# Performance work log

Measured on AMD Instinct MI355X. Metric: run time of the kernel, lower is better.

## Reference

```python
import jax, jax.numpy as jnp
import numpy as np
from jax import lax

T, B, D, H, L, NDIR = 512, 64, 512, 512, 3, 2

def _lengths():
    return 512 - 4 * np.arange(64)  # per-sequence lengths, non-increasing

def _qdq(w):
    # simulate dynamic int8 symmetric per-tensor weight quantization
    s = jnp.max(jnp.abs(w)) / 127.0
    return jnp.clip(jnp.round(w / s), -127, 127) * s

def setup_inputs() -> dict:
    key = jax.random.key(0)
    ks = jax.random.split(key, 9)
    lengths = _lengths()
    bs = np.array([(lengths > t).sum() for t in range(T)], dtype=np.int64)  # [T]
    pack_idx = np.concatenate([t * B + np.arange(bs[t]) for t in range(T)]).astype(np.int32)
    sc = 0.05
    data = jax.random.normal(ks[0], (int(bs.sum()), D), jnp.float32)
    h0 = jax.random.normal(ks[1], (L * NDIR, B, H), jnp.float32)
    c0 = jax.random.normal(ks[2], (L * NDIR, B, H), jnp.float32)
    w_ih0 = _qdq(jax.random.normal(ks[3], (NDIR, 4 * H, D)) * sc)
    w_hh0 = _qdq(jax.random.normal(ks[4], (NDIR, 4 * H, H)) * sc)
    b0 = jax.random.normal(ks[5], (NDIR, 4 * H)) * sc  # b_ih + b_hh combined
    w_ih_r = _qdq(jax.random.normal(ks[6], (L - 1, NDIR, 4 * H, NDIR * H)) * sc)
    w_hh_r = _qdq(jax.random.normal(ks[7], (L - 1, NDIR, 4 * H, H)) * sc)
    b_r = jax.random.normal(ks[8], (L - 1, NDIR, 4 * H)) * sc
    return {"data": data, "h0": h0, "c0": c0, "w_ih0": w_ih0, "w_hh0": w_hh0, "b0": b0,
            "w_ih_r": w_ih_r, "w_hh_r": w_hh_r, "b_r": b_r,
            "batch_sizes": jnp.asarray(bs), "pack_idx": jnp.asarray(pack_idx)}

def _run_dir(x, mask, h0, c0, w_ih, w_hh, b):
    # x: [T,B,in], mask: [T,B]; batch the input GEMM over all timesteps
    gx = jnp.einsum('tbd,gd->tbg', x, w_ih) + b  # [T,B,4H]
    def step(carry, inp):
        h, c = carry
        gx_t, m = inp
        gates = gx_t + h @ w_hh.T
        i, f, g, o = jnp.split(gates, 4, axis=-1)  # PyTorch gate order i,f,g,o
        c_new = jax.nn.sigmoid(f) * c + jax.nn.sigmoid(i) * jnp.tanh(g)
        h_new = jax.nn.sigmoid(o) * jnp.tanh(c_new)
        m = m[:, None]
        return (jnp.where(m, h_new, h), jnp.where(m, c_new, c)), jnp.where(m, h_new, h)
    (hT, cT), ys = lax.scan(step, (h0, c0), (gx, mask))
    return ys * mask[:, :, None], hT, cT

def _lstm(data, h0, c0, w_ih0, w_hh0, b0, w_ih_r, w_hh_r, b_r, batch_sizes, pack_idx):
    mask = jnp.arange(B)[None, :] < batch_sizes[:, None]          # [T,B] valid slots
    lengths = jnp.sum(mask, axis=0)                                # [B]
    rev_idx = jnp.clip(lengths[None, :] - 1 - jnp.arange(T)[:, None], 0, T - 1)  # [T,B]
    barange = jnp.arange(B)[None, :]
    x = jnp.zeros((T * B, D), data.dtype).at[pack_idx].set(data).reshape(T, B, D)
    h_ns, c_ns = [], []
    for l in range(L):
        outs = []
        for d in range(NDIR):
            if l == 0:
                w_ih, w_hh, b = w_ih0[d], w_hh0[d], b0[d]
            else:
                w_ih, w_hh, b = w_ih_r[l - 1, d], w_hh_r[l - 1, d], b_r[l - 1, d]
            hi, ci = h0[NDIR * l + d], c0[NDIR * l + d]
            if d == 0:
                ys, hT, cT = _run_dir(x, mask, hi, ci, w_ih, w_hh, b)
            else:
                x_rev = x[rev_idx, barange]               # per-sequence reversal
                ys_r, hT, cT = _run_dir(x_rev, mask, hi, ci, w_ih, w_hh, b)
                ys = ys_r[rev_idx, barange] * mask[:, :, None]
            outs.append(ys); h_ns.append(hT); c_ns.append(cT)
        x = jnp.concatenate(outs, axis=-1)  # [T,B,2H] feeds next layer
    out = x.reshape(T * B, NDIR * H)[pack_idx]  # repack to [total_tokens, 2H]
    return out, jnp.stack(h_ns), jnp.stack(c_ns)

def reference(data, h0, c0, w_ih0, w_hh0, b0, w_ih_r, w_hh_r, b_r, batch_sizes, pack_idx):
    return _lstm(data, h0, c0, w_ih0, w_hh0, b0, w_ih_r, w_hh_r, b_r, batch_sizes, pack_idx)
```

## Files before the change

### kernel.cpp

```cpp
#include <hip/hip_runtime.h>
#include <cmath>

typedef _Float16 f16;
typedef _Float16 half8 __attribute__((ext_vector_type(8)));
typedef float floatx4 __attribute__((ext_vector_type(4)));
typedef unsigned u32x4 __attribute__((ext_vector_type(4)));

#define NT 512
#define NB 64
#define NH 512
#define NG 2048
#define CHUNK 128

__device__ inline float sigf(float x) { return 1.0f / (1.0f + __expf(-x)); }
__device__ inline float tanhfast(float x) { return 2.0f / (1.0f + __expf(-2.0f * x)) - 1.0f; }

__device__ inline void load_lds16(const f16* g, f16* l) {
  __builtin_amdgcn_global_load_lds(
      (__attribute__((address_space(1))) void*)g,
      (__attribute__((address_space(3))) void*)l, 16, 0, 0);
}

__global__ void prep_meta(const int* __restrict__ bs_raw, int* __restrict__ lens,
                          int* __restrict__ cum) {
  __shared__ int sbs[NT];
  int stride = (bs_raw[1] == 0) ? 2 : 1;
  for (int i = threadIdx.x; i < NT; i += 256) sbs[i] = bs_raw[i * stride];
  __syncthreads();
  for (int b = threadIdx.x; b < NB; b += 256) {
    int n = 0;
    for (int t = 0; t < NT; ++t) n += (sbs[t] > b);
    lens[b] = n;
  }
  if (threadIdx.x == 0) {
    int run = 0;
    for (int t = 0; t < NT; ++t) { cum[t] = run; run += sbs[t]; }
  }
}

__global__ void scatter_rows(const float* __restrict__ data, const int* __restrict__ pidx,
                             f16* __restrict__ X0) {
  int r = blockIdx.x;
  int row = pidx[r];
  const float* src = data + (size_t)r * 512;
  f16* dst = X0 + (size_t)row * 512;
  for (int k = threadIdx.x; k < 512; k += 256) dst[k] = (f16)src[k];
}

__global__ void f32_to_f16(const float* __restrict__ in, f16* __restrict__ out, size_t n) {
  size_t i = (size_t)blockIdx.x * 256 + threadIdx.x;
  size_t stride = (size_t)gridDim.x * 256;
  for (; i < n; i += stride) out[i] = (f16)in[i];
}

__global__ void init_h(const float* __restrict__ h0, const float* __restrict__ c0,
                       float* __restrict__ hsave, float* __restrict__ csave,
                       unsigned* __restrict__ ht, unsigned* __restrict__ ctr, int layer) {
  int idx = blockIdx.x * 256 + threadIdx.x;
  int d = idx >> 15, rem = idx & 32767;
  float hv = h0[(size_t)(2 * layer + d) * NB * NH + rem];
  float cv = c0[(size_t)(2 * layer + d) * NB * NH + rem];
  hsave[idx] = hv;
  csave[idx] = cv;
  union { f16 f; unsigned short s; } hc; hc.f = (f16)hv;
  unsigned word = ((unsigned)(layer * NT) << 16) | hc.s;
  __hip_atomic_store(ht + (size_t)d * NB * NH + rem, word,
                     __ATOMIC_RELAXED, __HIP_MEMORY_SCOPE_AGENT);
  if (blockIdx.x == 0) {
    __hip_atomic_store(ctr + threadIdx.x, (unsigned)(layer * NT),
                       __ATOMIC_RELAXED, __HIP_MEMORY_SCOPE_AGENT);
  }
}

__device__ void gemm_body(const f16* __restrict__ A, const f16* __restrict__ W,
                          const float* __restrict__ bias, const int* __restrict__ lens,
                          f16* __restrict__ gxc, int K, int c0, int id) {
  const int d = id >> 10;
  const int m0 = ((id >> 4) & 63) * 128;
  const int n0 = (id & 15) * 128;
  const f16* Wd = W + (size_t)d * NG * K;

  __shared__ __align__(16) f16 As[128 * 32];
  __shared__ __align__(16) f16 Bs[128 * 32];

  const int tid = threadIdx.x, lane = tid & 63, wv = tid >> 6;
  const int wm = wv >> 1, wn = wv & 1;
  const int lrow = lane >> 2, lcol = (lane & 3) * 8;
  const int q = lane >> 4, nn = lane & 15;

  const f16* aptr[2];
  const f16* bptr[2];
#pragma unroll
  for (int i = 0; i < 2; ++i) {
    int ch = wv * 2 + i;
    int m = m0 + ch * 16 + lrow;
    int t = c0 + (m >> 6), b = m & 63;
    int tt = t;
    if (d) { tt = lens[b] - 1 - t; tt = tt < 0 ? 0 : (tt > NT - 1 ? NT - 1 : tt); }
    aptr[i] = A + (size_t)(tt * NB + b) * K + lcol;
    bptr[i] = Wd + (size_t)(n0 + ch * 16 + lrow) * K + lcol;
  }

  floatx4 acc[4][4] = {};
  for (int k0 = 0; k0 < K; k0 += 32) {
    __syncthreads();
#pragma unroll
    for (int i = 0; i < 2; ++i) {
      int ch = wv * 2 + i;
      load_lds16(aptr[i] + k0, As + ch * 512);
      load_lds16(bptr[i] + k0, Bs + ch * 512);
    }
    __syncthreads();
    half8 a[4], b[4];
#pragma unroll
    for (int f = 0; f < 4; ++f) {
      a[f] = *(const half8*)(As + (wm * 64 + f * 16 + nn) * 32 + q * 8);
      b[f] = *(const half8*)(Bs + (wn * 64 + f * 16 + nn) * 32 + q * 8);
    }
#pragma unroll
    for (int fm = 0; fm < 4; ++fm)
#pragma unroll
      for (int fn = 0; fn < 4; ++fn)
        acc[fm][fn] = __builtin_amdgcn_mfma_f32_16x16x32_f16(a[fm], b[fn], acc[fm][fn], 0, 0, 0);
  }

  f16* gxd = gxc + (size_t)d * CHUNK * NB * NG;
#pragma unroll
  for (int fn = 0; fn < 4; ++fn) {
    int col = n0 + wn * 64 + fn * 16 + nn;
    float bv = bias[d * NG + col];
#pragma unroll
    for (int fm = 0; fm < 4; ++fm) {
      int mb = m0 + wm * 64 + fm * 16 + q * 4;
#pragma unroll
      for (int r = 0; r < 4; ++r)
        gxd[(size_t)(mb + r) * NG + col] = (f16)(acc[fm][fn][r] + bv);
    }
  }
}

__global__ __launch_bounds__(256) void gemm_gx(const f16* __restrict__ A,
                                               const f16* __restrict__ W,
                                               const float* __restrict__ bias,
                                               const int* __restrict__ lens,
                                               f16* __restrict__ gxc, int K, int c0) {
  gemm_body(A, W, bias, lens, gxc, K, c0,
            (int)(blockIdx.z * 1024 + blockIdx.y * 16 + blockIdx.x));
}

__global__ __launch_bounds__(256, 1) void lstm_rec(
    const f16* __restrict__ gxc, const f16* __restrict__ whh,
    const int* __restrict__ lens, const int* __restrict__ cum,
    float* __restrict__ hsave, float* __restrict__ csave,
    unsigned* __restrict__ ht, unsigned* __restrict__ ctr,
    f16* __restrict__ Y, float* __restrict__ outp,
    float* __restrict__ hT, float* __restrict__ cT,
    int c0, int mode, int layer,
    const f16* __restrict__ Xg, const f16* __restrict__ wih,
    const float* __restrict__ biasg, f16* __restrict__ gxn, int Kg, int c0n) {
  if (blockIdx.x >= 256) {
    if (gxn) gemm_body(Xg, wih, biasg, lens, gxn, Kg, c0n, (int)blockIdx.x - 256);
    return;
  }
  const int tid = threadIdx.x, lane = tid & 63, wv = tid >> 6;
  const int g = blockIdx.x & 7, w = blockIdx.x >> 3;
  const int dir = g & 1, bsl = g >> 1;
  const int q = lane >> 4, nn = lane & 15;

  const int maxlen = lens[bsl * 16];
  int nst = maxlen - c0;
  if (nst <= 0) return;
  if (nst > CHUNK) nst = CHUNK;

  __shared__ __align__(16) unsigned As[2][16][260];
  __shared__ float s_g[4][16][17];

  const int jbase = w * 16 + wv * 4;
  const int coln = (nn >> 2) * NH + jbase + (nn & 3);
  const f16* whd = whh + (size_t)dir * NG * NH;
  half8 bf[16];
#pragma unroll
  for (int s = 0; s < 16; ++s) {
    bf[s] = *(const half8*)(whd + (size_t)coln * NH + s * 32 + q * 8);
    asm volatile("" : "+v"(bf[s]));
  }

  const int b_e = bsl * 16 + nn;
  const int jglob = jbase + q;
  const int lene = lens[b_e];
  const int brow = bsl * 16 + q * 4;
  const int lidx = (dir * NB + b_e) * NH + jglob;
  float h = hsave[lidx], c = csave[lidx];

  const f16* gxd = gxc + (size_t)dir * CHUNK * NB * NG;
  const int ebase = layer * NT;

  const unsigned* cslot = ctr + (size_t)g * 32 + (lane & 31);

  for (int ct = 0; ct < nst; ++ct) {
    const int t = c0 + ct;
    const int e = ebase + t;
    const int par = t & 1;

    float gxv[4];
#pragma unroll
    for (int r = 0; r < 4; ++r)
      gxv[r] = (float)gxd[(size_t)(ct * NB + brow + r) * NG + coln];

    {
      const unsigned* cp = cslot + par * 256;
      int it = 0;
      for (;;) {
        unsigned cv = __hip_atomic_load(cp, __ATOMIC_RELAXED, __HIP_MEMORY_SCOPE_AGENT);
        if (__ballot((int)cv >= e) == ~0ull) break;
        if (++it > 200000) break;
        __builtin_amdgcn_s_sleep(1);
      }
    }

    const unsigned long long* p64 =
        (const unsigned long long*)(ht + ((size_t)(par * 2 + dir) * NB + bsl * 16 + nn) * NH +
                                    wv * 128 + q * 8);
    unsigned long long wb[16];
    {
      int it = 0;
      for (;;) {
#pragma unroll
        for (int i = 0; i < 16; ++i)
          wb[i] = __hip_atomic_load(p64 + (i >> 2) * 16 + (i & 3), __ATOMIC_RELAXED,
                                    __HIP_MEMORY_SCOPE_AGENT);
        unsigned tg = 0xffffu;
#pragma unroll
        for (int i = 0; i < 16; ++i) {
          tg &= (unsigned)(wb[i] >> 16) & 0xffffu;
          tg &= (unsigned)(wb[i] >> 48);
        }
        if (__ballot(tg >= (unsigned)e) == ~0ull) break;
        if (++it > 50000) break;
        __builtin_amdgcn_s_sleep(1);
      }
    }

#pragma unroll
    for (int s = 0; s < 4; ++s) {
      unsigned d0 = (unsigned)(wb[4 * s + 0] & 0xffffu) | ((unsigned)(wb[4 * s + 0] >> 32) << 16);
      unsigned d1 = (unsigned)(wb[4 * s + 1] & 0xffffu) | ((unsigned)(wb[4 * s + 1] >> 32) << 16);
      unsigned d2 = (unsigned)(wb[4 * s + 2] & 0xffffu) | ((unsigned)(wb[4 * s + 2] >> 32) << 16);
      unsigned d3 = (unsigned)(wb[4 * s + 3] & 0xffffu) | ((unsigned)(wb[4 * s + 3] >> 32) << 16);
      *(u32x4*)&As[par][nn][wv * 64 + s * 16 + q * 4] = (u32x4){d0, d1, d2, d3};
    }
    __syncthreads();

    floatx4 acc0 = {0.f, 0.f, 0.f, 0.f}, acc1 = {0.f, 0.f, 0.f, 0.f};
#pragma unroll
    for (int s = 0; s < 8; ++s) {
      half8 a0 = *(const half8*)&As[par][nn][(2 * s) * 16 + q * 4];
      half8 a1 = *(const half8*)&As[par][nn][(2 * s + 1) * 16 + q * 4];
      acc0 = __builtin_amdgcn_mfma_f32_16x16x32_f16(a0, bf[2 * s], acc0, 0, 0, 0);
      acc1 = __builtin_amdgcn_mfma_f32_16x16x32_f16(a1, bf[2 * s + 1], acc1, 0, 0, 0);
    }
#pragma unroll
    for (int r4 = 0; r4 < 4; ++r4) s_g[wv][q * 4 + r4][nn] = acc0[r4] + acc1[r4] + gxv[r4];

    const bool act = (t < lene);
    if (act) {
      float gi = s_g[wv][nn][q];
      float gf = s_g[wv][nn][4 + q];
      float gg = s_g[wv][nn][8 + q];
      float go = s_g[wv][nn][12 + q];
      c = sigf(gf) * c + sigf(gi) * tanhfast(gg);
      h = sigf(go) * tanhfast(c);
    }
    union { f16 f; unsigned short s; } hc; hc.f = (f16)h;
    unsigned word = ((unsigned)(e + 1) << 16) | hc.s;
    __hip_atomic_store(ht + ((size_t)(((t + 1) & 1) * 2 + dir) * NB + b_e) * NH + jglob,
                       word, __ATOMIC_RELAXED, __HIP_MEMORY_SCOPE_AGENT);
    if (tid == 0)
      __hip_atomic_store(ctr + (size_t)(((t + 1) & 1) * 256 + g * 32 + w), (unsigned)(e + 1),
                         __ATOMIC_RELAXED, __HIP_MEMORY_SCOPE_AGENT);
    if (mode == 0) {
      int tp = act ? (dir ? (lene - 1 - t) : t) : t;
      Y[(size_t)(tp * NB + b_e) * (2 * NH) + dir * NH + jglob] = act ? (f16)h : (f16)0.f;
    } else if (act) {
      int tp = dir ? (lene - 1 - t) : t;
      outp[(size_t)(cum[tp] + b_e) * (2 * NH) + dir * NH + jglob] = h;
    }
  }

  hsave[lidx] = h;
  csave[lidx] = c;
  const int sidx = ((2 * layer + dir) * NB + b_e) * NH + jglob;
  hT[sidx] = h;
  cT[sidx] = c;
}

extern "C" void kernel_launch(void* const* d_in, const int* in_sizes, int n_in,
                              void* d_out, int out_size, void* d_ws, size_t ws_size,
                              hipStream_t stream) {
  const float* data  = (const float*)d_in[0];
  const float* h0    = (const float*)d_in[1];
  const float* c0    = (const float*)d_in[2];
  const float* w_ih0 = (const float*)d_in[3];
  const float* w_hh0 = (const float*)d_in[4];
  const float* b0    = (const float*)d_in[5];
  const float* w_ihr = (const float*)d_in[6];
  const float* w_hhr = (const float*)d_in[7];
  const float* b_r   = (const float*)d_in[8];
  const int* bs_raw  = (const int*)d_in[9];
  const int* pidx    = (const int*)d_in[10];
  const int nrows = in_sizes[0] / 512;
  float* out = (float*)d_out;

  f16* Y0 = (f16*)d_out;
  float* hT = out + (size_t)nrows * 1024;
  float* cT = hT + (size_t)6 * NB * NH;

  char* p = (char*)d_ws;
  auto take = [&](size_t bytes) {
    char* r = p;
    p += (bytes + 255) & ~(size_t)255;
    return (void*)r;
  };
  const size_t gsz = (size_t)2 * CHUNK * NB * NG * 2;
  f16* gxcA  = (f16*)take(gsz);
  f16* Y1    = (f16*)take((size_t)NT * NB * 1024 * 2);
  f16* X0    = Y1;
  f16* wih16 = (f16*)take((size_t)2 * NG * 1024 * 2);
  f16* whh16 = (f16*)take((size_t)2 * NG * NH * 2);
  unsigned* ht = (unsigned*)take((size_t)2 * 2 * NB * NH * 4);
  unsigned* ctr = (unsigned*)take((size_t)2 * 8 * 32 * 4);
  float* hsave = (float*)take((size_t)2 * NB * NH * 4);
  float* csave = (float*)take((size_t)2 * NB * NH * 4);
  int* lens = (int*)take(256);
  int* cum  = (int*)take(NT * 4);
  f16* gxcB = nullptr;
  if ((size_t)(p - (char*)d_ws) + gsz <= ws_size) gxcB = (f16*)take(gsz);
  const bool fuse = (gxcB != nullptr);

  prep_meta<<<1, 256, 0, stream>>>(bs_raw, lens, cum);
  (void)hipMemsetAsync(X0, 0, (size_t)NT * NB * 512 * 2, stream);
  (void)hipMemsetAsync(ht, 0, (size_t)2 * 2 * NB * NH * 4, stream);
  (void)hipMemsetAsync(ctr, 0, (size_t)2 * 8 * 32 * 4, stream);
  scatter_rows<<<nrows, 256, 0, stream>>>(data, pidx, X0);

  for (int l = 0; l < 3; ++l) {
    const float* wih_f = (l == 0) ? w_ih0 : w_ihr + (size_t)(l - 1) * 2 * NG * 1024;
    const float* whh_f = (l == 0) ? w_hh0 : w_hhr + (size_t)(l - 1) * 2 * NG * NH;
    const float* bias  = (l == 0) ? b0 : b_r + (size_t)(l - 1) * 2 * NG;
    const int K = (l == 0) ? 512 : 1024;
    const f16* Xl = (l == 0) ? X0 : ((l == 1) ? Y0 : Y1);
    f16* Yl = (l == 0) ? Y0 : Y1;
    f32_to_f16<<<256, 256, 0, stream>>>(wih_f, wih16, (size_t)2 * NG * K);
    f32_to_f16<<<256, 256, 0, stream>>>(whh_f, whh16, (size_t)2 * NG * NH);
    init_h<<<256, 256, 0, stream>>>(h0, c0, hsave, csave, ht, ctr, l);
    for (int c = 0; c < 4; ++c) {
      f16* gcur = fuse ? ((c & 1) ? gxcB : gxcA) : gxcA;
      if (c == 0 || !fuse)
        gemm_gx<<<dim3(16, 64, 2), 256, 0, stream>>>(Xl, wih16, bias, lens, gcur, K, c * CHUNK);
      const bool g_on = fuse && (c < 3);
      f16* gnext = g_on ? (((c + 1) & 1) ? gxcB : gxcA) : nullptr;
      const int grid = g_on ? 2304 : 256;
      lstm_rec<<<grid, 256, 0, stream>>>(gcur, whh16, lens, cum, hsave, csave, ht, ctr, Yl,
                                         out, hT, cT, c * CHUNK, (l == 2) ? 1 : 0, l,
                                         Xl, wih16, bias, gnext, K, (c + 1) * CHUNK);
    }
  }
}
```

Measured before the change: 6.990 ms.

## Share LDS between recurrent and GEMM blocks, raise recurrent priority, fuse prep kernels

The recurrent kernel's fused GEMM tail blocks and the recurrent blocks now alias a single shared-memory buffer instead of separate static arrays. This lowers the per-block LDS footprint so more GEMM blocks can be co-resident with the recurrent blocks. Recurrent blocks raise their wave priority with s_setprio so the latency-critical recurrence is scheduled ahead of the overlapping GEMM work. The three per-layer prep kernels (two weight conversions and h/c init) are merged into one launch to cut launch overhead.

```diff
diff --git a/kernel.cpp b/kernel.cpp
--- a/kernel.cpp
+++ b/kernel.cpp
@@ -47,41 +47,41 @@
   for (int k = threadIdx.x; k < 512; k += 256) dst[k] = (f16)src[k];
 }
 
-__global__ void f32_to_f16(const float* __restrict__ in, f16* __restrict__ out, size_t n) {
-  size_t i = (size_t)blockIdx.x * 256 + threadIdx.x;
-  size_t stride = (size_t)gridDim.x * 256;
-  for (; i < n; i += stride) out[i] = (f16)in[i];
-}
-
-__global__ void init_h(const float* __restrict__ h0, const float* __restrict__ c0,
-                       float* __restrict__ hsave, float* __restrict__ csave,
-                       unsigned* __restrict__ ht, unsigned* __restrict__ ctr, int layer) {
-  int idx = blockIdx.x * 256 + threadIdx.x;
-  int d = idx >> 15, rem = idx & 32767;
-  float hv = h0[(size_t)(2 * layer + d) * NB * NH + rem];
-  float cv = c0[(size_t)(2 * layer + d) * NB * NH + rem];
-  hsave[idx] = hv;
-  csave[idx] = cv;
-  union { f16 f; unsigned short s; } hc; hc.f = (f16)hv;
-  unsigned word = ((unsigned)(layer * NT) << 16) | hc.s;
-  __hip_atomic_store(ht + (size_t)d * NB * NH + rem, word,
-                     __ATOMIC_RELAXED, __HIP_MEMORY_SCOPE_AGENT);
-  if (blockIdx.x == 0) {
-    __hip_atomic_store(ctr + threadIdx.x, (unsigned)(layer * NT),
+__global__ void prep_layer(const float* __restrict__ wih_f, f16* __restrict__ wih16, int n1,
+                           const float* __restrict__ whh_f, f16* __restrict__ whh16, int n2,
+                           const float* __restrict__ h0, const float* __restrict__ c0,
+                           float* __restrict__ hsave, float* __restrict__ csave,
+                           unsigned* __restrict__ ht, unsigned* __restrict__ ctr, int layer) {
+  int gid = blockIdx.x * 256 + threadIdx.x;
+  int stride = gridDim.x * 256;
+  for (int i = gid; i < n1; i += stride) wih16[i] = (f16)wih_f[i];
+  for (int i = gid; i < n2; i += stride) whh16[i] = (f16)whh_f[i];
+  for (int i = gid; i < 2 * NB * NH; i += stride) {
+    int d = i >> 15, rem = i & 32767;
+    float hv = h0[(size_t)(2 * layer + d) * NB * NH + rem];
+    float cv = c0[(size_t)(2 * layer + d) * NB * NH + rem];
+    hsave[i] = hv;
+    csave[i] = cv;
+    union { f16 f; unsigned short s; } hc; hc.f = (f16)hv;
+    unsigned word = ((unsigned)(layer * NT) << 16) | hc.s;
+    __hip_atomic_store(ht + (size_t)d * NB * NH + rem, word,
                        __ATOMIC_RELAXED, __HIP_MEMORY_SCOPE_AGENT);
   }
+  if (gid < 256)
+    __hip_atomic_store(ctr + gid, (unsigned)(layer * NT),
+                       __ATOMIC_RELAXED, __HIP_MEMORY_SCOPE_AGENT);
 }
 
 __device__ void gemm_body(const f16* __restrict__ A, const f16* __restrict__ W,
                           const float* __restrict__ bias, const int* __restrict__ lens,
-                          f16* __restrict__ gxc, int K, int c0, int id) {
+                          f16* __restrict__ gxc, int K, int c0, int id, char* sm) {
   const int d = id >> 10;
   const int m0 = ((id >> 4) & 63) * 128;
   const int n0 = (id & 15) * 128;
   const f16* Wd = W + (size_t)d * NG * K;
 
-  __shared__ __align__(16) f16 As[128 * 32];
-  __shared__ __align__(16) f16 Bs[128 * 32];
+  f16* As = (f16*)sm;
+  f16* Bs = (f16*)(sm + 8192);
 
   const int tid = threadIdx.x, lane = tid & 63, wv = tid >> 6;
   const int wm = wv >> 1, wn = wv & 1;
@@ -144,8 +144,9 @@
                                                const float* __restrict__ bias,
                                                const int* __restrict__ lens,
                                                f16* __restrict__ gxc, int K, int c0) {
+  __shared__ __align__(16) char gsm[16384];
   gemm_body(A, W, bias, lens, gxc, K, c0,
-            (int)(blockIdx.z * 1024 + blockIdx.y * 16 + blockIdx.x));
+            (int)(blockIdx.z * 1024 + blockIdx.y * 16 + blockIdx.x), gsm);
 }
 
 __global__ __launch_bounds__(256, 1) void lstm_rec(
@@ -158,10 +159,15 @@
     int c0, int mode, int layer,
     const f16* __restrict__ Xg, const f16* __restrict__ wih,
     const float* __restrict__ biasg, f16* __restrict__ gxn, int Kg, int c0n) {
+  __shared__ __align__(16) char smem[37632];
   if (blockIdx.x >= 256) {
-    if (gxn) gemm_body(Xg, wih, biasg, lens, gxn, Kg, c0n, (int)blockIdx.x - 256);
+    if (gxn) gemm_body(Xg, wih, biasg, lens, gxn, Kg, c0n, (int)blockIdx.x - 256, smem);
     return;
   }
+  __builtin_amdgcn_s_setprio(1);
+  unsigned (*As)[16][260] = (unsigned(*)[16][260])smem;
+  float (*s_g)[16][17] = (float(*)[16][17])(smem + 33280);
+
   const int tid = threadIdx.x, lane = tid & 63, wv = tid >> 6;
   const int g = blockIdx.x & 7, w = blockIdx.x >> 3;
   const int dir = g & 1, bsl = g >> 1;
@@ -171,9 +177,6 @@
   int nst = maxlen - c0;
   if (nst <= 0) return;
   if (nst > CHUNK) nst = CHUNK;
-
-  __shared__ __align__(16) unsigned As[2][16][260];
-  __shared__ float s_g[4][16][17];
 
   const int jbase = w * 16 + wv * 4;
   const int coln = (nn >> 2) * NH + jbase + (nn & 3);
@@ -350,9 +353,8 @@
     const int K = (l == 0) ? 512 : 1024;
     const f16* Xl = (l == 0) ? X0 : ((l == 1) ? Y0 : Y1);
     f16* Yl = (l == 0) ? Y0 : Y1;
-    f32_to_f16<<<256, 256, 0, stream>>>(wih_f, wih16, (size_t)2 * NG * K);
-    f32_to_f16<<<256, 256, 0, stream>>>(whh_f, whh16, (size_t)2 * NG * NH);
-    init_h<<<256, 256, 0, stream>>>(h0, c0, hsave, csave, ht, ctr, l);
+    prep_layer<<<512, 256, 0, stream>>>(wih_f, wih16, 2 * NG * K, whh_f, whh16,
+                                        2 * NG * NH, h0, c0, hsave, csave, ht, ctr, l);
     for (int c = 0; c < 4; ++c) {
       f16* gcur = fuse ? ((c & 1) ? gxcB : gxcA) : gxcA;
       if (c == 0 || !fuse)
```

Result: faster. 6.826 ms (-2.3%).
